# Kernel optimization log

Hardware: AMD Instinct MI355X
Metric: run time of the kernel (lower is better)

The kernel has to match this reference:

```python
import jax, jax.numpy as jnp
import numpy as np

EPS = 1e-6          # epsilon for ray-triangle intersection
HIT_TOL = 1e-3      # hit tolerance for occlusion test (t < 1 - HIT_TOL)
MIN_LEN = 1.2e-6    # ~10 * float32 eps, minimal squared segment length


def _dot(u, v=None, keepdims=False):
    v = u if v is None else v
    return jnp.sum(u * v, axis=-1, keepdims=keepdims)


def _rays_intersect_triangles(ro, rd, tv):
    # Moller-Trumbore. ro/rd: [..., 3]; tv: [..., 3, 3] (broadcastable).
    v0 = tv[..., 0, :]
    e1 = tv[..., 1, :] - v0
    e2 = tv[..., 2, :] - v0
    h = jnp.cross(rd, e2)
    a = _dot(e1, h)
    cond_a = jnp.abs(a) < EPS
    f = jnp.where(cond_a, 0.0, 1.0 / jnp.where(cond_a, 1.0, a))
    s = ro - v0
    u = f * _dot(s, h)
    q = jnp.cross(s, e1)
    v = f * _dot(rd, q)
    t = f * _dot(e2, q)
    hit = (~cond_a) & (u >= 0.0) & (u <= 1.0) & (v >= 0.0) & (u + v <= 1.0) & (t > EPS)
    return t, hit


def _image_method(tx_b, rx_b, mirror_vertices, mirror_normals):
    # tx_b/rx_b: [T,R,P,3]; mirror_vertices/normals: [P,order,3]
    mv = jnp.moveaxis(mirror_vertices, 1, 0)  # [order,P,3]
    mn = jnp.moveaxis(mirror_normals, 1, 0)

    def fwd(carry, x):
        m_v, m_n = x
        img = carry - 2.0 * _dot(carry - m_v, m_n, keepdims=True) * m_n
        return img, img

    _, images = jax.lax.scan(fwd, tx_b, (mv, mn))

    def bwd(carry, x):
        m_v, m_n, img = x
        u = carry - img
        un = _dot(u, m_n, keepdims=True)
        vn = _dot(img - m_v, m_n, keepdims=True)
        bad = un == 0.0
        t = jnp.where(bad, 0.0, -vn / jnp.where(bad, 1.0, un))
        p = img + t * u
        return p, p

    _, paths = jax.lax.scan(bwd, rx_b, (mv, mn, images), reverse=True)
    return jnp.moveaxis(paths, 0, -2)  # [T,R,P,order,3]


def _forward(mesh_vertices, mesh_triangles, tx_vertices, rx_vertices, path_candidates):
    T, R = tx_vertices.shape[0], rx_vertices.shape[0]
    P, order = path_candidates.shape
    tv_all = mesh_vertices[mesh_triangles]  # [NF,3,3]
    fn = jnp.cross(tv_all[:, 1] - tv_all[:, 0], tv_all[:, 2] - tv_all[:, 0])
    normals = fn / jnp.linalg.norm(fn, axis=-1, keepdims=True)  # [NF,3]
    tri_v = tv_all[path_candidates]          # [P,order,3,3]
    mirror_vertices = tri_v[..., 0, :]       # [P,order,3]
    mirror_normals = normals[path_candidates]
    tx_b = jnp.broadcast_to(tx_vertices[:, None, None, :], (T, R, P, 3))
    rx_b = jnp.broadcast_to(rx_vertices[None, :, None, :], (T, R, P, 3))
    paths = _image_method(tx_b, rx_b, mirror_vertices, mirror_normals)
    full_paths = jnp.concatenate((tx_b[..., None, :], paths, rx_b[..., None, :]), axis=-2)  # [T,R,P,order+2,3]
    ro = full_paths[..., :-1, :]
    rd = jnp.diff(full_paths, axis=-2)
    # reflection points lie inside their triangles
    _, hit_in = _rays_intersect_triangles(ro[..., :-1, :], rd[..., :-1, :], tri_v)
    inside = hit_in.all(axis=-1)
    # consecutive vertices on same side of each mirror
    d_prev = _dot(full_paths[..., :-2, :] - mirror_vertices, mirror_normals)
    d_next = _dot(full_paths[..., 2:, :] - mirror_vertices, mirror_normals)
    valid_refl = (d_prev * d_next >= 0.0).all(axis=-1)
    # occlusion: any segment blocked by any triangle
    t_all, hit_all = _rays_intersect_triangles(ro[..., None, :], rd[..., None, :], tv_all)
    blocked = (hit_all & (t_all < 1.0 - HIT_TOL)).any(axis=-1).any(axis=-1)
    too_small = (_dot(rd) < MIN_LEN).any(axis=-1)
    mask = inside & valid_refl & (~blocked) & (~too_small)
    return full_paths, mask


def setup_inputs():
    key = jax.random.key(0)
    k1, k2, k3, k4, k5 = jax.random.split(key, 5)
    NV, NF, T, R, P, ORDER = 3000, 600, 2, 4, 1000, 2
    return {
        "mesh_vertices": jax.random.normal(k1, (NV, 3), dtype=jnp.float32),
        "mesh_triangles": jax.random.randint(k2, (NF, 3), 0, NV, dtype=jnp.int32),
        "tx_vertices": jax.random.normal(k3, (T, 3), dtype=jnp.float32),
        "rx_vertices": jax.random.normal(k4, (R, 3), dtype=jnp.float32),
        "path_candidates": jax.random.randint(k5, (P, ORDER), 0, NF, dtype=jnp.int32),
    }


def reference(mesh_vertices, mesh_triangles, tx_vertices, rx_vertices, path_candidates):
    full_paths, mask = _forward(mesh_vertices, mesh_triangles, tx_vertices, rx_vertices, path_candidates)
    T, R = tx_vertices.shape[0], rx_vertices.shape[0]
    P, order = path_candidates.shape
    dt = path_candidates.dtype
    tx_obj = jnp.broadcast_to(jnp.arange(T, dtype=dt)[:, None, None, None], (T, R, P, 1))
    rx_obj = jnp.broadcast_to(jnp.arange(R, dtype=dt)[None, :, None, None], (T, R, P, 1))
    pc = jnp.broadcast_to(path_candidates, (T, R, P, order))
    objects = jnp.concatenate((tx_obj, pc, rx_obj), axis=-1)
    return full_paths, objects, mask
```

## Files before the change

### kernel.cpp

```cpp
#include <hip/hip_runtime.h>


#define DEV __device__ __forceinline__

struct F3 { float x, y, z; };

DEV float fmul(float a, float b) { return __fmul_rn(a, b); }
DEV float fadd(float a, float b) { return __fadd_rn(a, b); }
DEV float fsub(float a, float b) { return __fsub_rn(a, b); }

DEV F3 f3sub(F3 a, F3 b) { return { fsub(a.x,b.x), fsub(a.y,b.y), fsub(a.z,b.z) }; }
DEV float f3dot(F3 a, F3 b) {
  return fadd(fadd(fmul(a.x,b.x), fmul(a.y,b.y)), fmul(a.z,b.z));
}
DEV F3 f3cross(F3 a, F3 b) {
  return { fsub(fmul(a.y,b.z), fmul(a.z,b.y)),
           fsub(fmul(a.z,b.x), fmul(a.x,b.z)),
           fsub(fmul(a.x,b.y), fmul(a.y,b.x)) };
}

struct MTRes { float t; bool hit; };

DEV MTRes mt(F3 ro, F3 rd, F3 v0, F3 e1, F3 e2) {
  F3 h = f3cross(rd, e2);
  float a = f3dot(e1, h);
  bool conda = fabsf(a) < 1e-6f;
  float f = conda ? 0.0f : __fdiv_rn(1.0f, a);
  F3 s = f3sub(ro, v0);
  float u = fmul(f, f3dot(s, h));
  F3 q = f3cross(s, e1);
  float v = fmul(f, f3dot(rd, q));
  float tt = fmul(f, f3dot(e2, q));
  bool hit = (!conda) && (u >= 0.0f) && (u <= 1.0f) && (v >= 0.0f)
             && (fadd(u, v) <= 1.0f) && (tt > 1e-6f);
  return { tt, hit };
}

__global__ void k_pretri(const float* __restrict__ verts, const int* __restrict__ tris,
                         float4* __restrict__ out, int nf) {
  int f = blockIdx.x * blockDim.x + threadIdx.x;
  if (f >= nf) return;
  int i0 = tris[3*f+0], i1 = tris[3*f+1], i2 = tris[3*f+2];
  F3 v0 = { verts[3*i0], verts[3*i0+1], verts[3*i0+2] };
  F3 v1 = { verts[3*i1], verts[3*i1+1], verts[3*i1+2] };
  F3 v2 = { verts[3*i2], verts[3*i2+1], verts[3*i2+2] };
  F3 e1 = f3sub(v1, v0);
  F3 e2 = f3sub(v2, v0);
  F3 fn = f3cross(e1, e2);
  float nrm = __fsqrt_rn(fadd(fadd(fmul(fn.x,fn.x), fmul(fn.y,fn.y)), fmul(fn.z,fn.z)));
  F3 n = { __fdiv_rn(fn.x, nrm), __fdiv_rn(fn.y, nrm), __fdiv_rn(fn.z, nrm) };
  out[3*f+0] = make_float4(v0.x, v0.y, v0.z, e1.x);
  out[3*f+1] = make_float4(e1.y, e1.z, e2.x, e2.y);
  out[3*f+2] = make_float4(e2.z, n.x, n.y, n.z);
}

__global__ __launch_bounds__(256) void k_paths(
    const float* __restrict__ txv, const float* __restrict__ rxv,
    const int* __restrict__ pc, const float4* __restrict__ tri,
    float* __restrict__ out, int T, int R, int P, int nf)
{
  const int lane = threadIdx.x & 63;
  const int pw = blockIdx.x * 4 + (threadIdx.x >> 6);
  const int nPaths = T * R * P;
  if (pw >= nPaths) return;
  const int p  = pw % P;
  const int tr = pw / P;
  const int r  = tr % R;
  const int t  = tr / R;

  const int f0 = pc[2*p + 0];
  const int f1 = pc[2*p + 1];
  float4 a0 = tri[3*f0], b0 = tri[3*f0+1], c0 = tri[3*f0+2];
  float4 a1 = tri[3*f1], b1 = tri[3*f1+1], c1 = tri[3*f1+2];
  F3 v00 = {a0.x,a0.y,a0.z}, e10 = {a0.w,b0.x,b0.y}, e20 = {b0.z,b0.w,c0.x}, n0 = {c0.y,c0.z,c0.w};
  F3 v01 = {a1.x,a1.y,a1.z}, e11 = {a1.w,b1.x,b1.y}, e21 = {b1.z,b1.w,c1.x}, n1 = {c1.y,c1.z,c1.w};

  F3 TX = { txv[3*t], txv[3*t+1], txv[3*t+2] };
  F3 RX = { rxv[3*r], rxv[3*r+1], rxv[3*r+2] };

  float d0  = f3dot(f3sub(TX, v00), n0);
  float td0 = fmul(2.0f, d0);
  F3 img1 = { fsub(TX.x, fmul(td0, n0.x)), fsub(TX.y, fmul(td0, n0.y)), fsub(TX.z, fmul(td0, n0.z)) };
  float d1  = f3dot(f3sub(img1, v01), n1);
  float td1 = fmul(2.0f, d1);
  F3 img2 = { fsub(img1.x, fmul(td1, n1.x)), fsub(img1.y, fmul(td1, n1.y)), fsub(img1.z, fmul(td1, n1.z)) };

  F3 u2 = f3sub(RX, img2);
  float un = f3dot(u2, n1);
  float vn = f3dot(f3sub(img2, v01), n1);
  float tb = (un == 0.0f) ? 0.0f : __fdiv_rn(-vn, un);
  F3 p1 = { fadd(img2.x, fmul(tb, u2.x)), fadd(img2.y, fmul(tb, u2.y)), fadd(img2.z, fmul(tb, u2.z)) };

  F3 u1 = f3sub(p1, img1);
  un = f3dot(u1, n0);
  vn = f3dot(f3sub(img1, v00), n0);
  tb = (un == 0.0f) ? 0.0f : __fdiv_rn(-vn, un);
  F3 p0 = { fadd(img1.x, fmul(tb, u1.x)), fadd(img1.y, fmul(tb, u1.y)), fadd(img1.z, fmul(tb, u1.z)) };

  F3 ro0 = TX, ro1 = p0, ro2 = p1;
  F3 rd0 = f3sub(p0, TX), rd1 = f3sub(p1, p0), rd2 = f3sub(RX, p1);

  MTRes h0 = mt(ro0, rd0, v00, e10, e20);
  MTRes h1 = mt(ro1, rd1, v01, e11, e21);
  bool inside = h0.hit && h1.hit;

  float dp0 = f3dot(f3sub(TX, v00), n0);
  float dn0 = f3dot(f3sub(p1, v00), n0);
  float dp1 = f3dot(f3sub(p0, v01), n1);
  float dn1 = f3dot(f3sub(RX, v01), n1);
  bool vrefl = (fmul(dp0, dn0) >= 0.0f) && (fmul(dp1, dn1) >= 0.0f);

  bool toosmall = (f3dot(rd0, rd0) < 1.2e-6f) ||
                  (f3dot(rd1, rd1) < 1.2e-6f) ||
                  (f3dot(rd2, rd2) < 1.2e-6f);

  bool pre = inside && vrefl && !toosmall;
  bool blocked = false;
  if (pre) {
    for (int base = 0; base < nf; base += 64) {
      const int f = base + lane;
      bool blk = false;
      if (f < nf) {
        float4 aa = tri[3*f], bb = tri[3*f+1], cc = tri[3*f+2];
        F3 w0  = {aa.x, aa.y, aa.z};
        F3 we1 = {aa.w, bb.x, bb.y};
        F3 we2 = {bb.z, bb.w, cc.x};
        MTRes hb0 = mt(ro0, rd0, w0, we1, we2);
        MTRes hb1 = mt(ro1, rd1, w0, we1, we2);
        MTRes hb2 = mt(ro2, rd2, w0, we1, we2);
        blk = (hb0.hit && (hb0.t < 0.999f))
           || (hb1.hit && (hb1.t < 0.999f))
           || (hb2.hit && (hb2.t < 0.999f));
      }
      if (__ballot(blk) != 0ULL) { blocked = true; break; }
    }
  }
  bool mask = pre && !blocked;

  if (lane == 0) {
    float4* fp = reinterpret_cast<float4*>(out) + (size_t)pw * 3;
    fp[0] = make_float4(TX.x, TX.y, TX.z, p0.x);
    fp[1] = make_float4(p0.y, p0.z, p1.x, p1.y);
    fp[2] = make_float4(p1.z, RX.x, RX.y, RX.z);
    float4* ob = reinterpret_cast<float4*>(out + (size_t)nPaths * 12) + pw;
    *ob = make_float4((float)t, (float)f0, (float)f1, (float)r);
    out[(size_t)nPaths * 16 + pw] = mask ? 1.0f : 0.0f;
  }
}

extern "C" void kernel_launch(void* const* d_in, const int* in_sizes, int n_in,
                              void* d_out, int out_size, void* d_ws, size_t ws_size,
                              hipStream_t stream) {
  const float* mesh_v = (const float*)d_in[0];
  const int*   mesh_t = (const int*)d_in[1];
  const float* txv    = (const float*)d_in[2];
  const float* rxv    = (const float*)d_in[3];
  const int*   pc     = (const int*)d_in[4];

  const int NF = in_sizes[1] / 3;
  const int T  = in_sizes[2] / 3;
  const int R  = in_sizes[3] / 3;
  const int P  = in_sizes[4] / 2;

  float4* tris = (float4*)d_ws;

  k_pretri<<<(NF + 255) / 256, 256, 0, stream>>>(mesh_v, mesh_t, tris, NF);

  const int nPaths = T * R * P;
  const int blocks = (nPaths + 3) / 4;
  k_paths<<<blocks, 256, 0, stream>>>(txv, rxv, pc, tris, (float*)d_out,
                                      T, R, P, NF);
}
```

Before: 69.15 us.

## Split path prefilter from occlusion test and compact surviving paths

Path construction and the cheap validity checks now run one thread per path, with no longer one 64-lane wave per path. Surviving paths are compacted into a workspace list through an atomic counter. A separate grid-stride occlusion kernel then assigns one wave to each surviving path and tests it against all triangles. This is meant to stop launching a full wave for every path when most are rejected before the occlusion loop, at the cost of an extra kernel launch, atomics, and record traffic through global memory.

```diff
diff --git a/kernel.cpp b/kernel.cpp
--- a/kernel.cpp
+++ b/kernel.cpp
@@ -37,8 +37,9 @@
 }
 
 __global__ void k_pretri(const float* __restrict__ verts, const int* __restrict__ tris,
-                         float4* __restrict__ out, int nf) {
+                         float4* __restrict__ out, int* __restrict__ counter, int nf) {
   int f = blockIdx.x * blockDim.x + threadIdx.x;
+  if (f == 0) *counter = 0;
   if (f >= nf) return;
   int i0 = tris[3*f+0], i1 = tris[3*f+1], i2 = tris[3*f+2];
   F3 v0 = { verts[3*i0], verts[3*i0+1], verts[3*i0+2] };
@@ -54,13 +55,13 @@
   out[3*f+2] = make_float4(e2.z, n.x, n.y, n.z);
 }
 
-__global__ __launch_bounds__(256) void k_paths(
+__global__ __launch_bounds__(256) void k_prefilter(
     const float* __restrict__ txv, const float* __restrict__ rxv,
     const int* __restrict__ pc, const float4* __restrict__ tri,
-    float* __restrict__ out, int T, int R, int P, int nf)
+    float4* __restrict__ srec, int* __restrict__ counter,
+    float* __restrict__ out, int T, int R, int P)
 {
-  const int lane = threadIdx.x & 63;
-  const int pw = blockIdx.x * 4 + (threadIdx.x >> 6);
+  const int pw = blockIdx.x * blockDim.x + threadIdx.x;
   const int nPaths = T * R * P;
   if (pw >= nPaths) return;
   const int p  = pw % P;
@@ -115,8 +116,47 @@
                   (f3dot(rd2, rd2) < 1.2e-6f);
 
   bool pre = inside && vrefl && !toosmall;
-  bool blocked = false;
+
+  float4* fp = reinterpret_cast<float4*>(out) + (size_t)pw * 3;
+  fp[0] = make_float4(TX.x, TX.y, TX.z, p0.x);
+  fp[1] = make_float4(p0.y, p0.z, p1.x, p1.y);
+  fp[2] = make_float4(p1.z, RX.x, RX.y, RX.z);
+  float4* ob = reinterpret_cast<float4*>(out + (size_t)nPaths * 12) + pw;
+  *ob = make_float4((float)t, (float)f0, (float)f1, (float)r);
+  out[(size_t)nPaths * 16 + pw] = pre ? 1.0f : 0.0f;
+
   if (pre) {
+    int idx = atomicAdd(counter, 1);
+    float4* rec = srec + (size_t)idx * 5;
+    rec[0] = make_float4(ro0.x, ro0.y, ro0.z, ro1.x);
+    rec[1] = make_float4(ro1.y, ro1.z, ro2.x, ro2.y);
+    rec[2] = make_float4(ro2.z, rd0.x, rd0.y, rd0.z);
+    rec[3] = make_float4(rd1.x, rd1.y, rd1.z, rd2.x);
+    rec[4] = make_float4(rd2.y, rd2.z, __int_as_float(pw), 0.0f);
+  }
+}
+
+__global__ __launch_bounds__(256) void k_occl(
+    const float4* __restrict__ tri, const float4* __restrict__ srec,
+    const int* __restrict__ counter, float* __restrict__ out,
+    int nPaths, int nf)
+{
+  const int lane = threadIdx.x & 63;
+  const int wid  = blockIdx.x * 4 + (threadIdx.x >> 6);
+  const int nW   = gridDim.x * 4;
+  const int S    = *counter;
+
+  for (int sid = wid; sid < S; sid += nW) {
+    const float4 r0 = srec[(size_t)sid*5+0];
+    const float4 r1 = srec[(size_t)sid*5+1];
+    const float4 r2 = srec[(size_t)sid*5+2];
+    const float4 r3 = srec[(size_t)sid*5+3];
+    const float4 r4 = srec[(size_t)sid*5+4];
+    F3 ro0 = {r0.x, r0.y, r0.z}, ro1 = {r0.w, r1.x, r1.y}, ro2 = {r1.z, r1.w, r2.x};
+    F3 rd0 = {r2.y, r2.z, r2.w}, rd1 = {r3.x, r3.y, r3.z}, rd2 = {r3.w, r4.x, r4.y};
+    const int pw = __float_as_int(r4.z);
+
+    bool blocked = false;
     for (int base = 0; base < nf; base += 64) {
       const int f = base + lane;
       bool blk = false;
@@ -134,17 +174,7 @@
       }
       if (__ballot(blk) != 0ULL) { blocked = true; break; }
     }
-  }
-  bool mask = pre && !blocked;
-
-  if (lane == 0) {
-    float4* fp = reinterpret_cast<float4*>(out) + (size_t)pw * 3;
-    fp[0] = make_float4(TX.x, TX.y, TX.z, p0.x);
-    fp[1] = make_float4(p0.y, p0.z, p1.x, p1.y);
-    fp[2] = make_float4(p1.z, RX.x, RX.y, RX.z);
-    float4* ob = reinterpret_cast<float4*>(out + (size_t)nPaths * 12) + pw;
-    *ob = make_float4((float)t, (float)f0, (float)f1, (float)r);
-    out[(size_t)nPaths * 16 + pw] = mask ? 1.0f : 0.0f;
+    if (blocked && lane == 0) out[(size_t)nPaths * 16 + pw] = 0.0f;
   }
 }
 
@@ -161,13 +191,17 @@
   const int T  = in_sizes[2] / 3;
   const int R  = in_sizes[3] / 3;
   const int P  = in_sizes[4] / 2;
-
-  float4* tris = (float4*)d_ws;
-
-  k_pretri<<<(NF + 255) / 256, 256, 0, stream>>>(mesh_v, mesh_t, tris, NF);
-
   const int nPaths = T * R * P;
-  const int blocks = (nPaths + 3) / 4;
-  k_paths<<<blocks, 256, 0, stream>>>(txv, rxv, pc, tris, (float*)d_out,
-                                      T, R, P, NF);
-}
+
+  char* ws = (char*)d_ws;
+  float4* tris    = (float4*)ws;
+  int*    counter = (int*)(ws + 32768);
+  float4* srec    = (float4*)(ws + 36864);
+
+  k_pretri<<<(NF + 255) / 256, 256, 0, stream>>>(mesh_v, mesh_t, tris, counter, NF);
+
+  k_prefilter<<<(nPaths + 255) / 256, 256, 0, stream>>>(
+      txv, rxv, pc, tris, srec, counter, (float*)d_out, T, R, P);
+
+  k_occl<<<512, 256, 0, stream>>>(tris, srec, counter, (float*)d_out, nPaths, NF);
+}
```

Result: no change. 68.16 us (-1.4%).

## Fuse triangle precompute into path kernel with shared-memory triangles and compacted occlusion

Applied to the files above, without the earlier changes.

Drops the separate triangle-precompute launch. Each block now builds the full triangle table (vertex plus edges) in shared memory, and one thread computes each path, recomputing normals for its two mirror faces. Paths that pass the validity tests are compacted through a shared atomic counter, and the four wavefronts then run the occlusion test only for those rays against the shared-memory triangles. The aim is to save a launch and a global-memory round trip and to avoid wasting wavefronts on invalid paths. In exchange, every block redundantly rebuilds the triangle table, and MAXF caps the face count at 1024, beyond which shared memory overflows.

```diff
diff --git a/kernel.cpp b/kernel.cpp
--- a/kernel.cpp
+++ b/kernel.cpp
@@ -2,6 +2,8 @@
 
 
 #define DEV __device__ __forceinline__
+#define MAXF 1024
+#define PPB  64
 
 struct F3 { float x, y, z; };
 
@@ -36,95 +38,137 @@
   return { tt, hit };
 }
 
-__global__ void k_pretri(const float* __restrict__ verts, const int* __restrict__ tris,
-                         float4* __restrict__ out, int nf) {
-  int f = blockIdx.x * blockDim.x + threadIdx.x;
-  if (f >= nf) return;
-  int i0 = tris[3*f+0], i1 = tris[3*f+1], i2 = tris[3*f+2];
-  F3 v0 = { verts[3*i0], verts[3*i0+1], verts[3*i0+2] };
-  F3 v1 = { verts[3*i1], verts[3*i1+1], verts[3*i1+2] };
-  F3 v2 = { verts[3*i2], verts[3*i2+1], verts[3*i2+2] };
-  F3 e1 = f3sub(v1, v0);
-  F3 e2 = f3sub(v2, v0);
-  F3 fn = f3cross(e1, e2);
-  float nrm = __fsqrt_rn(fadd(fadd(fmul(fn.x,fn.x), fmul(fn.y,fn.y)), fmul(fn.z,fn.z)));
-  F3 n = { __fdiv_rn(fn.x, nrm), __fdiv_rn(fn.y, nrm), __fdiv_rn(fn.z, nrm) };
-  out[3*f+0] = make_float4(v0.x, v0.y, v0.z, e1.x);
-  out[3*f+1] = make_float4(e1.y, e1.z, e2.x, e2.y);
-  out[3*f+2] = make_float4(e2.z, n.x, n.y, n.z);
-}
-
-__global__ __launch_bounds__(256) void k_paths(
+__global__ __launch_bounds__(256) void k_fused(
+    const float* __restrict__ verts, const int* __restrict__ tris,
     const float* __restrict__ txv, const float* __restrict__ rxv,
-    const int* __restrict__ pc, const float4* __restrict__ tri,
-    float* __restrict__ out, int T, int R, int P, int nf)
+    const int* __restrict__ pc, float* __restrict__ out,
+    int T, int R, int P, int nf)
 {
-  const int lane = threadIdx.x & 63;
-  const int pw = blockIdx.x * 4 + (threadIdx.x >> 6);
+  __shared__ float s_tri[MAXF * 9];
+  __shared__ float s_ray[PPB * 18];
+  __shared__ int   s_pw[PPB];
+  __shared__ int   s_cnt;
+
+  const int tid = threadIdx.x;
+  if (tid == 0) s_cnt = 0;
+
+  for (int f = tid; f < nf; f += 256) {
+    int i0 = tris[3*f+0], i1 = tris[3*f+1], i2 = tris[3*f+2];
+    F3 v0 = { verts[3*i0], verts[3*i0+1], verts[3*i0+2] };
+    F3 v1 = { verts[3*i1], verts[3*i1+1], verts[3*i1+2] };
+    F3 v2 = { verts[3*i2], verts[3*i2+1], verts[3*i2+2] };
+    F3 e1 = f3sub(v1, v0);
+    F3 e2 = f3sub(v2, v0);
+    float* d = s_tri + f * 9;
+    d[0] = v0.x; d[1] = v0.y; d[2] = v0.z;
+    d[3] = e1.x; d[4] = e1.y; d[5] = e1.z;
+    d[6] = e2.x; d[7] = e2.y; d[8] = e2.z;
+  }
+  __syncthreads();
+
   const int nPaths = T * R * P;
-  if (pw >= nPaths) return;
-  const int p  = pw % P;
-  const int tr = pw / P;
-  const int r  = tr % R;
-  const int t  = tr / R;
-
-  const int f0 = pc[2*p + 0];
-  const int f1 = pc[2*p + 1];
-  float4 a0 = tri[3*f0], b0 = tri[3*f0+1], c0 = tri[3*f0+2];
-  float4 a1 = tri[3*f1], b1 = tri[3*f1+1], c1 = tri[3*f1+2];
-  F3 v00 = {a0.x,a0.y,a0.z}, e10 = {a0.w,b0.x,b0.y}, e20 = {b0.z,b0.w,c0.x}, n0 = {c0.y,c0.z,c0.w};
-  F3 v01 = {a1.x,a1.y,a1.z}, e11 = {a1.w,b1.x,b1.y}, e21 = {b1.z,b1.w,c1.x}, n1 = {c1.y,c1.z,c1.w};
-
-  F3 TX = { txv[3*t], txv[3*t+1], txv[3*t+2] };
-  F3 RX = { rxv[3*r], rxv[3*r+1], rxv[3*r+2] };
-
-  float d0  = f3dot(f3sub(TX, v00), n0);
-  float td0 = fmul(2.0f, d0);
-  F3 img1 = { fsub(TX.x, fmul(td0, n0.x)), fsub(TX.y, fmul(td0, n0.y)), fsub(TX.z, fmul(td0, n0.z)) };
-  float d1  = f3dot(f3sub(img1, v01), n1);
-  float td1 = fmul(2.0f, d1);
-  F3 img2 = { fsub(img1.x, fmul(td1, n1.x)), fsub(img1.y, fmul(td1, n1.y)), fsub(img1.z, fmul(td1, n1.z)) };
-
-  F3 u2 = f3sub(RX, img2);
-  float un = f3dot(u2, n1);
-  float vn = f3dot(f3sub(img2, v01), n1);
-  float tb = (un == 0.0f) ? 0.0f : __fdiv_rn(-vn, un);
-  F3 p1 = { fadd(img2.x, fmul(tb, u2.x)), fadd(img2.y, fmul(tb, u2.y)), fadd(img2.z, fmul(tb, u2.z)) };
-
-  F3 u1 = f3sub(p1, img1);
-  un = f3dot(u1, n0);
-  vn = f3dot(f3sub(img1, v00), n0);
-  tb = (un == 0.0f) ? 0.0f : __fdiv_rn(-vn, un);
-  F3 p0 = { fadd(img1.x, fmul(tb, u1.x)), fadd(img1.y, fmul(tb, u1.y)), fadd(img1.z, fmul(tb, u1.z)) };
-
-  F3 ro0 = TX, ro1 = p0, ro2 = p1;
-  F3 rd0 = f3sub(p0, TX), rd1 = f3sub(p1, p0), rd2 = f3sub(RX, p1);
-
-  MTRes h0 = mt(ro0, rd0, v00, e10, e20);
-  MTRes h1 = mt(ro1, rd1, v01, e11, e21);
-  bool inside = h0.hit && h1.hit;
-
-  float dp0 = f3dot(f3sub(TX, v00), n0);
-  float dn0 = f3dot(f3sub(p1, v00), n0);
-  float dp1 = f3dot(f3sub(p0, v01), n1);
-  float dn1 = f3dot(f3sub(RX, v01), n1);
-  bool vrefl = (fmul(dp0, dn0) >= 0.0f) && (fmul(dp1, dn1) >= 0.0f);
-
-  bool toosmall = (f3dot(rd0, rd0) < 1.2e-6f) ||
-                  (f3dot(rd1, rd1) < 1.2e-6f) ||
-                  (f3dot(rd2, rd2) < 1.2e-6f);
-
-  bool pre = inside && vrefl && !toosmall;
-  bool blocked = false;
-  if (pre) {
+  const int pw = blockIdx.x * PPB + tid;
+
+  if (tid < PPB && pw < nPaths) {
+    const int p  = pw % P;
+    const int tr = pw / P;
+    const int r  = tr % R;
+    const int t  = tr / R;
+
+    const int f0 = pc[2*p + 0];
+    const int f1 = pc[2*p + 1];
+    const float* t0 = s_tri + f0 * 9;
+    const float* t1 = s_tri + f1 * 9;
+    F3 v00 = {t0[0],t0[1],t0[2]}, e10 = {t0[3],t0[4],t0[5]}, e20 = {t0[6],t0[7],t0[8]};
+    F3 v01 = {t1[0],t1[1],t1[2]}, e11 = {t1[3],t1[4],t1[5]}, e21 = {t1[6],t1[7],t1[8]};
+
+    F3 fn0 = f3cross(e10, e20);
+    float nrm0 = __fsqrt_rn(f3dot(fn0, fn0));
+    F3 n0 = { __fdiv_rn(fn0.x, nrm0), __fdiv_rn(fn0.y, nrm0), __fdiv_rn(fn0.z, nrm0) };
+    F3 fn1 = f3cross(e11, e21);
+    float nrm1 = __fsqrt_rn(f3dot(fn1, fn1));
+    F3 n1 = { __fdiv_rn(fn1.x, nrm1), __fdiv_rn(fn1.y, nrm1), __fdiv_rn(fn1.z, nrm1) };
+
+    F3 TX = { txv[3*t], txv[3*t+1], txv[3*t+2] };
+    F3 RX = { rxv[3*r], rxv[3*r+1], rxv[3*r+2] };
+
+    float d0  = f3dot(f3sub(TX, v00), n0);
+    float td0 = fmul(2.0f, d0);
+    F3 img1 = { fsub(TX.x, fmul(td0, n0.x)), fsub(TX.y, fmul(td0, n0.y)), fsub(TX.z, fmul(td0, n0.z)) };
+    float d1  = f3dot(f3sub(img1, v01), n1);
+    float td1 = fmul(2.0f, d1);
+    F3 img2 = { fsub(img1.x, fmul(td1, n1.x)), fsub(img1.y, fmul(td1, n1.y)), fsub(img1.z, fmul(td1, n1.z)) };
+
+    F3 u2 = f3sub(RX, img2);
+    float un = f3dot(u2, n1);
+    float vn = f3dot(f3sub(img2, v01), n1);
+    float tb = (un == 0.0f) ? 0.0f : __fdiv_rn(-vn, un);
+    F3 p1 = { fadd(img2.x, fmul(tb, u2.x)), fadd(img2.y, fmul(tb, u2.y)), fadd(img2.z, fmul(tb, u2.z)) };
+
+    F3 u1 = f3sub(p1, img1);
+    un = f3dot(u1, n0);
+    vn = f3dot(f3sub(img1, v00), n0);
+    tb = (un == 0.0f) ? 0.0f : __fdiv_rn(-vn, un);
+    F3 p0 = { fadd(img1.x, fmul(tb, u1.x)), fadd(img1.y, fmul(tb, u1.y)), fadd(img1.z, fmul(tb, u1.z)) };
+
+    F3 ro0 = TX, ro1 = p0, ro2 = p1;
+    F3 rd0 = f3sub(p0, TX), rd1 = f3sub(p1, p0), rd2 = f3sub(RX, p1);
+
+    MTRes h0 = mt(ro0, rd0, v00, e10, e20);
+    MTRes h1 = mt(ro1, rd1, v01, e11, e21);
+    bool inside = h0.hit && h1.hit;
+
+    float dp0 = f3dot(f3sub(TX, v00), n0);
+    float dn0 = f3dot(f3sub(p1, v00), n0);
+    float dp1 = f3dot(f3sub(p0, v01), n1);
+    float dn1 = f3dot(f3sub(RX, v01), n1);
+    bool vrefl = (fmul(dp0, dn0) >= 0.0f) && (fmul(dp1, dn1) >= 0.0f);
+
+    bool toosmall = (f3dot(rd0, rd0) < 1.2e-6f) ||
+                    (f3dot(rd1, rd1) < 1.2e-6f) ||
+                    (f3dot(rd2, rd2) < 1.2e-6f);
+
+    bool pre = inside && vrefl && !toosmall;
+
+    float4* fp = reinterpret_cast<float4*>(out) + (size_t)pw * 3;
+    fp[0] = make_float4(TX.x, TX.y, TX.z, p0.x);
+    fp[1] = make_float4(p0.y, p0.z, p1.x, p1.y);
+    fp[2] = make_float4(p1.z, RX.x, RX.y, RX.z);
+    float4* ob = reinterpret_cast<float4*>(out + (size_t)nPaths * 12) + pw;
+    *ob = make_float4((float)t, (float)f0, (float)f1, (float)r);
+    out[(size_t)nPaths * 16 + pw] = pre ? 1.0f : 0.0f;
+
+    if (pre) {
+      int idx = atomicAdd(&s_cnt, 1);
+      float* rr = s_ray + idx * 18;
+      rr[0]=ro0.x;  rr[1]=ro0.y;  rr[2]=ro0.z;
+      rr[3]=ro1.x;  rr[4]=ro1.y;  rr[5]=ro1.z;
+      rr[6]=ro2.x;  rr[7]=ro2.y;  rr[8]=ro2.z;
+      rr[9]=rd0.x;  rr[10]=rd0.y; rr[11]=rd0.z;
+      rr[12]=rd1.x; rr[13]=rd1.y; rr[14]=rd1.z;
+      rr[15]=rd2.x; rr[16]=rd2.y; rr[17]=rd2.z;
+      s_pw[idx] = pw;
+    }
+  }
+  __syncthreads();
+
+  const int S = s_cnt;
+  const int lane = tid & 63;
+  const int wid  = tid >> 6;
+  for (int s = wid; s < S; s += 4) {
+    const float* rr = s_ray + s * 18;
+    F3 ro0 = {rr[0],rr[1],rr[2]},   ro1 = {rr[3],rr[4],rr[5]},   ro2 = {rr[6],rr[7],rr[8]};
+    F3 rd0 = {rr[9],rr[10],rr[11]}, rd1 = {rr[12],rr[13],rr[14]}, rd2 = {rr[15],rr[16],rr[17]};
+
+    bool blocked = false;
     for (int base = 0; base < nf; base += 64) {
       const int f = base + lane;
       bool blk = false;
       if (f < nf) {
-        float4 aa = tri[3*f], bb = tri[3*f+1], cc = tri[3*f+2];
-        F3 w0  = {aa.x, aa.y, aa.z};
-        F3 we1 = {aa.w, bb.x, bb.y};
-        F3 we2 = {bb.z, bb.w, cc.x};
+        const float* tt = s_tri + f * 9;
+        F3 w0  = {tt[0], tt[1], tt[2]};
+        F3 we1 = {tt[3], tt[4], tt[5]};
+        F3 we2 = {tt[6], tt[7], tt[8]};
         MTRes hb0 = mt(ro0, rd0, w0, we1, we2);
         MTRes hb1 = mt(ro1, rd1, w0, we1, we2);
         MTRes hb2 = mt(ro2, rd2, w0, we1, we2);
@@ -134,17 +178,7 @@
       }
       if (__ballot(blk) != 0ULL) { blocked = true; break; }
     }
-  }
-  bool mask = pre && !blocked;
-
-  if (lane == 0) {
-    float4* fp = reinterpret_cast<float4*>(out) + (size_t)pw * 3;
-    fp[0] = make_float4(TX.x, TX.y, TX.z, p0.x);
-    fp[1] = make_float4(p0.y, p0.z, p1.x, p1.y);
-    fp[2] = make_float4(p1.z, RX.x, RX.y, RX.z);
-    float4* ob = reinterpret_cast<float4*>(out + (size_t)nPaths * 12) + pw;
-    *ob = make_float4((float)t, (float)f0, (float)f1, (float)r);
-    out[(size_t)nPaths * 16 + pw] = mask ? 1.0f : 0.0f;
+    if (blocked && lane == 0) out[(size_t)(T*R*P) * 16 + s_pw[s]] = 0.0f;
   }
 }
 
@@ -161,13 +195,9 @@
   const int T  = in_sizes[2] / 3;
   const int R  = in_sizes[3] / 3;
   const int P  = in_sizes[4] / 2;
-
-  float4* tris = (float4*)d_ws;
-
-  k_pretri<<<(NF + 255) / 256, 256, 0, stream>>>(mesh_v, mesh_t, tris, NF);
-
   const int nPaths = T * R * P;
-  const int blocks = (nPaths + 3) / 4;
-  k_paths<<<blocks, 256, 0, stream>>>(txv, rxv, pc, tris, (float*)d_out,
-                                      T, R, P, NF);
-}
+
+  const int blocks = (nPaths + PPB - 1) / PPB;
+  k_fused<<<blocks, 256, 0, stream>>>(mesh_v, mesh_t, txv, rxv, pc,
+                                      (float*)d_out, T, R, P, NF);
+}
```

Result: faster. 64.22 us (median of 2 runs) (-7.1%).
